# Kernel tuning notes

Hardware: AMD Instinct MI355X
Metric: run time of the kernel (lower is better)

The kernel has to match this reference:

```python
import jax, jax.numpy as jnp
import numpy as np

B, N, D, H = 4, 2048, 1024, 16
DK = D // H
LAMBDA = 0.5


def _linear_params(key, fan_in, fan_out):
    kw, kb = jax.random.split(key)
    bound = 1.0 / np.sqrt(fan_in)
    W = jax.random.uniform(kw, (fan_in, fan_out), jnp.float32, -bound, bound)
    b = jax.random.uniform(kb, (fan_out,), jnp.float32, -bound, bound)
    return W, b


def setup_inputs() -> dict:
    key = jax.random.key(0)
    ks = jax.random.split(key, 10)
    x = jax.random.normal(ks[0], (B, N, D), jnp.float32)
    # binary DAG-like adjacency (sparse-ish)
    causal_graph = jax.random.bernoulli(ks[1], 0.05, (N, N)).astype(jnp.float32)
    # differentiable backdoor mask: exp(-lambda*|Z|), 0 where no valid backdoor set
    Z = jax.random.randint(ks[2], (N, N), 0, 6).astype(jnp.float32)
    exists = jax.random.bernoulli(ks[3], 0.8, (N, N)).astype(jnp.float32)
    backdoor_mask = jnp.exp(-LAMBDA * Z) * exists
    Wq, bq = _linear_params(ks[4], D, D)
    Wk, bk = _linear_params(ks[5], D, D)
    Wc, bc = _linear_params(ks[6], N, D)  # W_cause: n_variables -> d_model
    We, be = _linear_params(ks[7], N, D)  # W_effect: n_variables -> d_model
    Wv, bv = _linear_params(ks[8], D, D)
    Wo, bo = _linear_params(ks[9], D, D)
    return dict(x=x, causal_graph=causal_graph, backdoor_mask=backdoor_mask,
                Wq=Wq, bq=bq, Wk=Wk, bk=bk, Wc=Wc, bc=bc, We=We, be=be,
                Wv=Wv, bv=bv, Wo=Wo, bo=bo)


def reference(x, causal_graph, backdoor_mask, Wq, bq, Wk, bk, Wc, bc, We, be, Wv, bv, Wo, bo):
    # Formula 5: asymmetric causal Q/K projections
    Q = x @ Wq + bq + (causal_graph @ Wc + bc)[None]        # [B,N,D]
    K = x @ Wk + bk + (causal_graph.T @ We + be)[None]      # [B,N,D]
    V = x @ Wv + bv                                          # [B,N,D]
    Qh = Q.reshape(B, N, H, DK)
    Kh = K.reshape(B, N, H, DK)
    Vh = V.reshape(B, N, H, DK)
    scores = jnp.einsum('bihd,bjhd->bhij', Qh, Kh) / np.sqrt(DK).astype(np.float32)
    # backdoor mask is MULTIPLICATIVE on raw scores (pre-softmax)
    scores = scores * backdoor_mask[None, None]
    attn = jax.nn.softmax(scores, axis=-1)                  # [B,H,N,N]
    out = jnp.einsum('bhij,bjhd->bihd', attn, Vh).reshape(B, N, D)
    return out @ Wo + bo
```

## Files before the change

kernel.cpp:

```cpp
#include <hip/hip_runtime.h>
#include <hip/hip_bf16.h>

#define BB 4
#define NN 2048
#define DD 1024
#define HH 16

using bf16 = __hip_bfloat16;
typedef __attribute__((ext_vector_type(8))) short bf16x8s;
typedef __attribute__((ext_vector_type(4))) float f32x4;

#define GLOAD_LDS16(gp, lp)                                                   \
  __builtin_amdgcn_global_load_lds(                                           \
      (const __attribute__((address_space(1))) void*)(gp),                    \
      (__attribute__((address_space(3))) void*)(lp), 16, 0, 0)

__global__ void cast_f32_bf16(const float* __restrict__ in, bf16* __restrict__ out, int n) {
  int i = (blockIdx.x * blockDim.x + threadIdx.x) * 4;
  if (i >= n) return;
  float4 v = *reinterpret_cast<const float4*>(in + i);
  ushort4 o;
  bf16 t0 = __float2bfloat16(v.x); o.x = *reinterpret_cast<unsigned short*>(&t0);
  bf16 t1 = __float2bfloat16(v.y); o.y = *reinterpret_cast<unsigned short*>(&t1);
  bf16 t2 = __float2bfloat16(v.z); o.z = *reinterpret_cast<unsigned short*>(&t2);
  bf16 t3 = __float2bfloat16(v.w); o.w = *reinterpret_cast<unsigned short*>(&t3);
  *reinterpret_cast<ushort4*>(out + i) = o;
}

__device__ __forceinline__ void transpose_tile(const float* __restrict__ in,
                                               bf16* __restrict__ out, int R, int C) {
  __shared__ float t[32][33];
  int c0 = blockIdx.x * 32, r0 = blockIdx.y * 32;
  int tx = threadIdx.x, ty = threadIdx.y;
#pragma unroll
  for (int i = 0; i < 4; i++)
    t[ty + i * 8][tx] = in[(size_t)(r0 + ty + i * 8) * C + c0 + tx];
  __syncthreads();
#pragma unroll
  for (int i = 0; i < 4; i++)
    out[(size_t)(c0 + ty + i * 8) * R + r0 + tx] = __float2bfloat16(t[tx][ty + i * 8]);
}

__global__ void transpose_cast4(const float* __restrict__ W0, const float* __restrict__ W1,
                                const float* __restrict__ W2, const float* __restrict__ W3,
                                bf16* __restrict__ O0, bf16* __restrict__ O1,
                                bf16* __restrict__ O2, bf16* __restrict__ O3) {
  const float* in; bf16* out;
  switch (blockIdx.z) {
    case 0: in = W0; out = O0; break;
    case 1: in = W1; out = O1; break;
    case 2: in = W2; out = O2; break;
    default: in = W3; out = O3; break;
  }
  transpose_tile(in, out, DD, DD);
}

__global__ void transpose_cast2(const float* __restrict__ W0, const float* __restrict__ W1,
                                bf16* __restrict__ O0, bf16* __restrict__ O1) {
  const float* in = blockIdx.z ? W1 : W0;
  bf16* out = blockIdx.z ? O1 : O0;
  transpose_tile(in, out, NN, DD);
}

__global__ void cg_prep(const float* __restrict__ in, bf16* __restrict__ outN,
                        bf16* __restrict__ outT) {
  __shared__ float t[32][33];
  int c0 = blockIdx.x * 32, r0 = blockIdx.y * 32;
  int tx = threadIdx.x, ty = threadIdx.y;
#pragma unroll
  for (int i = 0; i < 4; i++) {
    float v = in[(size_t)(r0 + ty + i * 8) * NN + c0 + tx];
    t[ty + i * 8][tx] = v;
    outN[(size_t)(r0 + ty + i * 8) * NN + c0 + tx] = __float2bfloat16(v);
  }
  __syncthreads();
#pragma unroll
  for (int i = 0; i < 4; i++)
    outT[(size_t)(c0 + ty + i * 8) * NN + r0 + tx] = __float2bfloat16(t[tx][ty + i * 8]);
}

__global__ void transpose_v(const bf16* __restrict__ Vb, bf16* __restrict__ Vt) {
  __shared__ short t[32][33];
  int bh = blockIdx.z; int b = bh >> 4, h = bh & 15;
  int n0 = blockIdx.x * 32, d0 = blockIdx.y * 32;
  int tx = threadIdx.x, ty = threadIdx.y;
#pragma unroll
  for (int i = 0; i < 4; i++)
    t[ty + i * 8][tx] = reinterpret_cast<const short*>(Vb)[
        (size_t)(b * NN + n0 + ty + i * 8) * DD + h * 64 + d0 + tx];
  __syncthreads();
#pragma unroll
  for (int i = 0; i < 4; i++)
    reinterpret_cast<short*>(Vt)[(size_t)(bh * 64 + d0 + ty + i * 8) * NN + n0 + tx] =
        t[tx][ty + i * 8];
}

template <int OUT_BF16, int HAS_ROWADD>
__device__ __forceinline__ void gemm_tile(
    const bf16* __restrict__ A, const bf16* __restrict__ BT, void* __restrict__ Cout,
    const float* __restrict__ bias, const float* __restrict__ rowadd,
    int Nc, int K, float scale, int brow, int bcol, short* As, short* Bs) {
  const int tid = threadIdx.x;
  const int l = tid & 63, w = tid >> 6;
  const int wr = (w >> 1) * 64, wc = (w & 1) * 64;
  const int lr = l & 15, lg = l >> 4;
  const int swz = lr & 7;
  f32x4 acc[4][4] = {};
  for (int k0 = 0; k0 < K; k0 += 64) {
#pragma unroll
    for (int i = 0; i < 4; i++) {
      int c = i * 256 + tid;
      int row = c >> 3, gch = (c & 7) ^ (row & 7);
      short* lA = As + (size_t)(i * 256 + w * 64) * 8;
      GLOAD_LDS16(A + (size_t)(brow + row) * K + k0 + gch * 8, lA);
      short* lB = Bs + (size_t)(i * 256 + w * 64) * 8;
      GLOAD_LDS16(BT + (size_t)(bcol + row) * K + k0 + gch * 8, lB);
    }
    __syncthreads();
#pragma unroll
    for (int t = 0; t < 2; t++) {
      bf16x8s a[4], bfr[4];
#pragma unroll
      for (int m = 0; m < 4; m++)
        a[m] = *reinterpret_cast<const bf16x8s*>(
            &As[(wr + m * 16 + lr) * 64 + ((t * 4 + lg) ^ swz) * 8]);
#pragma unroll
      for (int n = 0; n < 4; n++)
        bfr[n] = *reinterpret_cast<const bf16x8s*>(
            &Bs[(wc + n * 16 + lr) * 64 + ((t * 4 + lg) ^ swz) * 8]);
#pragma unroll
      for (int m = 0; m < 4; m++)
#pragma unroll
        for (int n = 0; n < 4; n++)
          acc[m][n] = __builtin_amdgcn_mfma_f32_16x16x32_bf16(a[m], bfr[n], acc[m][n], 0, 0, 0);
    }
    __syncthreads();
  }
#pragma unroll
  for (int m = 0; m < 4; m++) {
#pragma unroll
    for (int n = 0; n < 4; n++) {
      int col = bcol + wc + n * 16 + lr;
      float bv = bias[col];
#pragma unroll
      for (int r = 0; r < 4; r++) {
        int row = brow + wr + m * 16 + lg * 4 + r;
        float v = acc[m][n][r] + bv;
        if (HAS_ROWADD) v += rowadd[(size_t)(row & (NN - 1)) * Nc + col];
        v *= scale;
        if (OUT_BF16)
          reinterpret_cast<bf16*>(Cout)[(size_t)row * Nc + col] = __float2bfloat16(v);
        else
          reinterpret_cast<float*>(Cout)[(size_t)row * Nc + col] = v;
      }
    }
  }
}

template <int OUT_BF16, int HAS_ROWADD>
__global__ __launch_bounds__(256) void gemm_bt(
    const bf16* __restrict__ A, const bf16* __restrict__ BT, void* __restrict__ Cout,
    const float* __restrict__ bias, const float* __restrict__ rowadd,
    int M, int Nc, int K, float scale) {
  __shared__ short As[128 * 64];
  __shared__ short Bs[128 * 64];
  const int nbx = gridDim.x;
  const int nwg = nbx * gridDim.y;
  const int wg = blockIdx.y * nbx + blockIdx.x;
  const int swg = (wg & 7) * (nwg >> 3) + (wg >> 3);
  const int bxi = swg % nbx, byi = swg / nbx;
  gemm_tile<OUT_BF16, HAS_ROWADD>(A, BT, Cout, bias, rowadd, Nc, K, scale,
                                  byi * 128, bxi * 128, As, Bs);
}

__global__ __launch_bounds__(256) void gemm_dual(
    const bf16* __restrict__ A0, const bf16* __restrict__ B0, float* __restrict__ C0,
    const float* __restrict__ bias0,
    const bf16* __restrict__ A1, const bf16* __restrict__ B1, float* __restrict__ C1,
    const float* __restrict__ bias1, int Nc, int K) {
  __shared__ short As[128 * 64];
  __shared__ short Bs[128 * 64];
  const int nbx = gridDim.x;
  const int nwg = nbx * gridDim.y;
  const int wg = blockIdx.y * nbx + blockIdx.x;
  const int swg = (wg & 7) * (nwg >> 3) + (wg >> 3);
  const int bxi = swg % nbx, byi = swg / nbx;
  if (blockIdx.z == 0)
    gemm_tile<0, 0>(A0, B0, C0, bias0, nullptr, Nc, K, 1.0f, byi * 128, bxi * 128, As, Bs);
  else
    gemm_tile<0, 0>(A1, B1, C1, bias1, nullptr, Nc, K, 1.0f, byi * 128, bxi * 128, As, Bs);
}

__global__ __launch_bounds__(512, 4) void attn_k(
    const bf16* __restrict__ Qb, const bf16* __restrict__ Kb, const bf16* __restrict__ Vt,
    const float* __restrict__ mask, bf16* __restrict__ Ob) {
  constexpr int PPAD = 72;
  __shared__ short Ks[64 * 64];
  __shared__ short Vts[64 * 64];
  __shared__ short Ps[8][16 * PPAD];
  const int tid = threadIdx.x;
  const int wg = blockIdx.x;
  const int x = wg & 7, i = wg >> 3;
  const int b = x >> 1;
  const int h = ((x & 1) << 3) | (i & 7);
  const int q0 = ((i >> 3) & 15) * 128;
  const int l = tid & 63, w = tid >> 6;
  const int lr = l & 15, lg = l >> 4, lk = lg * 8;
  const int swz = lr & 7;

  const size_t qoff = (size_t)(b * NN + q0 + w * 16 + lr) * DD + h * 64;
  bf16x8s qf0 = *reinterpret_cast<const bf16x8s*>(Qb + qoff + lk);
  bf16x8s qf1 = *reinterpret_cast<const bf16x8s*>(Qb + qoff + 32 + lk);

  f32x4 acc[4] = {};
  float mrun = -1e30f, lrun = 0.f;

  const size_t kbase = (size_t)b * NN * DD + h * 64;
  const size_t vbase = (size_t)(b * HH + h) * 64 * NN;
  const float* mptr = mask + (size_t)(q0 + w * 16 + lr) * NN + lg * 4;

  const int r0 = tid >> 3, ch0 = tid & 7;
  const bf16* kg0 = Kb + kbase + (size_t)r0 * DD + ch0 * 8;
  const bf16* vg0 = Vt + vbase + (size_t)r0 * NN + ch0 * 8;
  short* kw0 = &Ks[r0 * 64 + (ch0 ^ (r0 & 7)) * 8];
  short* vw0 = &Vts[r0 * 64 + (ch0 ^ (r0 & 7)) * 8];

  uint4 kr0, vr0;
  kr0 = *reinterpret_cast<const uint4*>(kg0);
  vr0 = *reinterpret_cast<const uint4*>(vg0);

  for (int jt = 0; jt < NN; jt += 64) {
    __syncthreads();
    *reinterpret_cast<uint4*>(kw0) = kr0;
    *reinterpret_cast<uint4*>(vw0) = vr0;
    float4 m0 = *reinterpret_cast<const float4*>(mptr + jt + 0);
    float4 m1 = *reinterpret_cast<const float4*>(mptr + jt + 16);
    float4 m2 = *reinterpret_cast<const float4*>(mptr + jt + 32);
    float4 m3 = *reinterpret_cast<const float4*>(mptr + jt + 48);
    if (jt + 64 < NN) {
      kr0 = *reinterpret_cast<const uint4*>(kg0 + (size_t)(jt + 64) * DD);
      vr0 = *reinterpret_cast<const uint4*>(vg0 + jt + 64);
    }
    __syncthreads();

    f32x4 s[4];
#pragma unroll
    for (int jj = 0; jj < 4; jj++) {
      bf16x8s k0 = *reinterpret_cast<const bf16x8s*>(
          &Ks[(jj * 16 + lr) * 64 + ((0 + lg) ^ swz) * 8]);
      bf16x8s k1 = *reinterpret_cast<const bf16x8s*>(
          &Ks[(jj * 16 + lr) * 64 + ((4 + lg) ^ swz) * 8]);
      f32x4 z = {0.f, 0.f, 0.f, 0.f};
      z = __builtin_amdgcn_mfma_f32_16x16x32_bf16(k0, qf0, z, 0, 0, 0);
      s[jj] = __builtin_amdgcn_mfma_f32_16x16x32_bf16(k1, qf1, z, 0, 0, 0);
    }

    float lv[4][4];
    lv[0][0] = s[0][0] * m0.x; lv[0][1] = s[0][1] * m0.y;
    lv[0][2] = s[0][2] * m0.z; lv[0][3] = s[0][3] * m0.w;
    lv[1][0] = s[1][0] * m1.x; lv[1][1] = s[1][1] * m1.y;
    lv[1][2] = s[1][2] * m1.z; lv[1][3] = s[1][3] * m1.w;
    lv[2][0] = s[2][0] * m2.x; lv[2][1] = s[2][1] * m2.y;
    lv[2][2] = s[2][2] * m2.z; lv[2][3] = s[2][3] * m2.w;
    lv[3][0] = s[3][0] * m3.x; lv[3][1] = s[3][1] * m3.y;
    lv[3][2] = s[3][2] * m3.z; lv[3][3] = s[3][3] * m3.w;

    float mx0 = fmaxf(fmaxf(lv[0][0], lv[0][1]), fmaxf(lv[0][2], lv[0][3]));
    float mx1 = fmaxf(fmaxf(lv[1][0], lv[1][1]), fmaxf(lv[1][2], lv[1][3]));
    float mx2 = fmaxf(fmaxf(lv[2][0], lv[2][1]), fmaxf(lv[2][2], lv[2][3]));
    float mx3 = fmaxf(fmaxf(lv[3][0], lv[3][1]), fmaxf(lv[3][2], lv[3][3]));
    float mx = fmaxf(fmaxf(mx0, mx1), fmaxf(mx2, mx3));
    mx = fmaxf(mx, __shfl_xor(mx, 16, 64));
    mx = fmaxf(mx, __shfl_xor(mx, 32, 64));

    if (__any(mx > mrun + 11.0f)) {
      float mnew = fmaxf(mrun, mx);
      float sc = __builtin_amdgcn_exp2f(mrun - mnew);
      mrun = mnew;
      lrun *= sc;
#pragma unroll
      for (int s4 = 0; s4 < 4; s4++)
#pragma unroll
        for (int r = 0; r < 4; r++) acc[s4][r] *= sc;
    }

    short* Pw = &Ps[w][0];
    float rs = 0.f;
#pragma unroll
    for (int jj = 0; jj < 4; jj++) {
      float p0 = __builtin_amdgcn_exp2f(lv[jj][0] - mrun);
      float p1 = __builtin_amdgcn_exp2f(lv[jj][1] - mrun);
      float p2 = __builtin_amdgcn_exp2f(lv[jj][2] - mrun);
      float p3 = __builtin_amdgcn_exp2f(lv[jj][3] - mrun);
      rs += (p0 + p1) + (p2 + p3);
      ushort4 pk;
      bf16 b0 = __float2bfloat16(p0); pk.x = *reinterpret_cast<unsigned short*>(&b0);
      bf16 b1 = __float2bfloat16(p1); pk.y = *reinterpret_cast<unsigned short*>(&b1);
      bf16 b2 = __float2bfloat16(p2); pk.z = *reinterpret_cast<unsigned short*>(&b2);
      bf16 b3 = __float2bfloat16(p3); pk.w = *reinterpret_cast<unsigned short*>(&b3);
      *reinterpret_cast<ushort4*>(&Pw[lr * PPAD + jj * 16 + lg * 4]) = pk;
    }
    rs += __shfl_xor(rs, 16, 64);
    rs += __shfl_xor(rs, 32, 64);
    lrun += rs;

    asm volatile("s_waitcnt lgkmcnt(0)" ::: "memory");
    __builtin_amdgcn_sched_barrier(0);

    bf16x8s pb0 = *reinterpret_cast<const bf16x8s*>(&Pw[lr * PPAD + lk]);
    bf16x8s pb1 = *reinterpret_cast<const bf16x8s*>(&Pw[lr * PPAD + 32 + lk]);
#pragma unroll
    for (int s4 = 0; s4 < 4; s4++) {
      bf16x8s v0 = *reinterpret_cast<const bf16x8s*>(
          &Vts[(s4 * 16 + lr) * 64 + ((0 + lg) ^ swz) * 8]);
      bf16x8s v1 = *reinterpret_cast<const bf16x8s*>(
          &Vts[(s4 * 16 + lr) * 64 + ((4 + lg) ^ swz) * 8]);
      acc[s4] = __builtin_amdgcn_mfma_f32_16x16x32_bf16(v0, pb0, acc[s4], 0, 0, 0);
      acc[s4] = __builtin_amdgcn_mfma_f32_16x16x32_bf16(v1, pb1, acc[s4], 0, 0, 0);
    }
  }

  float rl = __builtin_amdgcn_rcpf(lrun);
  const size_t orow = (size_t)(b * NN + q0 + w * 16 + lr) * DD + h * 64;
#pragma unroll
  for (int s4 = 0; s4 < 4; s4++) {
    ushort4 o;
    bf16 b0 = __float2bfloat16(acc[s4][0] * rl); o.x = *reinterpret_cast<unsigned short*>(&b0);
    bf16 b1 = __float2bfloat16(acc[s4][1] * rl); o.y = *reinterpret_cast<unsigned short*>(&b1);
    bf16 b2 = __float2bfloat16(acc[s4][2] * rl); o.z = *reinterpret_cast<unsigned short*>(&b2);
    bf16 b3 = __float2bfloat16(acc[s4][3] * rl); o.w = *reinterpret_cast<unsigned short*>(&b3);
    *reinterpret_cast<ushort4*>(reinterpret_cast<unsigned short*>(Ob) + orow + s4 * 16 + lg * 4) = o;
  }
}

extern "C" void kernel_launch(void* const* d_in, const int* in_sizes, int n_in,
                              void* d_out, int out_size, void* d_ws, size_t ws_size,
                              hipStream_t stream) {
  (void)in_sizes; (void)n_in; (void)out_size; (void)ws_size;
  const float* x    = (const float*)d_in[0];
  const float* cg   = (const float*)d_in[1];
  const float* mask = (const float*)d_in[2];
  const float* Wq   = (const float*)d_in[3];
  const float* bq   = (const float*)d_in[4];
  const float* Wk   = (const float*)d_in[5];
  const float* bk   = (const float*)d_in[6];
  const float* Wc   = (const float*)d_in[7];
  const float* bc   = (const float*)d_in[8];
  const float* We   = (const float*)d_in[9];
  const float* be   = (const float*)d_in[10];
  const float* Wv   = (const float*)d_in[11];
  const float* bv   = (const float*)d_in[12];
  const float* Wo   = (const float*)d_in[13];
  const float* bo   = (const float*)d_in[14];

  auto MB = [](size_t m) { return m << 20; };
  char* ws = (char*)d_ws;
  bf16* xb   = (bf16*)(ws + MB(0));
  bf16* WqT  = (bf16*)(ws + MB(16));
  bf16* WkT  = (bf16*)(ws + MB(18));
  bf16* WvT  = (bf16*)(ws + MB(20));
  bf16* WoT  = (bf16*)(ws + MB(22));
  float* cq  = (float*)(ws + MB(24));
  float* ck  = (float*)(ws + MB(32));
  bf16* Qb   = (bf16*)(ws + MB(40));
  bf16* Kb   = (bf16*)(ws + MB(56));
  bf16* Vb   = (bf16*)(ws + MB(72));
  bf16* Vt   = (bf16*)(ws + MB(88));
  bf16* Ob   = (bf16*)(ws + MB(72));
  bf16* WcT  = (bf16*)(ws + MB(40));
  bf16* WeT  = (bf16*)(ws + MB(44));
  bf16* cgb  = (bf16*)(ws + MB(48));
  bf16* cgT  = (bf16*)(ws + MB(56));

  cast_f32_bf16<<<dim3(BB * NN * DD / 4 / 256), 256, 0, stream>>>(x, xb, BB * NN * DD);
  dim3 tb(32, 8);
  cg_prep<<<dim3(NN / 32, NN / 32), tb, 0, stream>>>(cg, cgb, cgT);
  transpose_cast4<<<dim3(DD / 32, DD / 32, 4), tb, 0, stream>>>(
      Wq, Wk, Wv, Wo, WqT, WkT, WvT, WoT);
  transpose_cast2<<<dim3(DD / 32, NN / 32, 2), tb, 0, stream>>>(Wc, We, WcT, WeT);

  gemm_dual<<<dim3(DD / 128, NN / 128, 2), 256, 0, stream>>>(
      cgb, WcT, cq, bc, cgT, WeT, ck, be, DD, NN);
  gemm_bt<1, 1><<<dim3(DD / 128, BB * NN / 128), 256, 0, stream>>>(
      xb, WqT, Qb, bq, cq, BB * NN, DD, DD, 0.125f * 1.4426950408889634f);
  gemm_bt<1, 1><<<dim3(DD / 128, BB * NN / 128), 256, 0, stream>>>(
      xb, WkT, Kb, bk, ck, BB * NN, DD, DD, 1.0f);
  gemm_bt<1, 0><<<dim3(DD / 128, BB * NN / 128), 256, 0, stream>>>(
      xb, WvT, Vb, bv, nullptr, BB * NN, DD, DD, 1.0f);

  transpose_v<<<dim3(NN / 32, 2, BB * HH), tb, 0, stream>>>(Vb, Vt);

  attn_k<<<dim3(NN / 128 * HH * BB), 512, 0, stream>>>(Qb, Kb, Vt, mask, Ob);

  gemm_bt<0, 0><<<dim3(DD / 128, BB * NN / 128), 256, 0, stream>>>(
      Ob, WoT, (float*)d_out, bo, nullptr, BB * NN, DD, DD, 1.0f);
}
```

Baseline: 310.8 us.

## Process two 16-row query tiles per wave in attention kernel

Each wave in the attention kernel now handles 32 query rows as two independent 16-row online-softmax streams, so each workgroup covers 256 queries and the grid is halved. Every K/V tile staged in shared memory is reused across twice as many queries, which cuts K/V global traffic and sync overhead per query. In exchange, register use roughly doubles (launch bounds drop from 4 to 2 waves-per-EU hint), occupancy falls, and there are only 512 workgroups.

Result: slower. 356.2 us (+14.6%).

```diff
diff --git a/kernel.cpp b/kernel.cpp
--- a/kernel.cpp
+++ b/kernel.cpp
@@ -191,33 +191,38 @@
     gemm_tile<0, 0>(A1, B1, C1, bias1, nullptr, Nc, K, 1.0f, byi * 128, bxi * 128, As, Bs);
 }
 
-__global__ __launch_bounds__(512, 4) void attn_k(
+__global__ __launch_bounds__(512, 2) void attn_k(
     const bf16* __restrict__ Qb, const bf16* __restrict__ Kb, const bf16* __restrict__ Vt,
     const float* __restrict__ mask, bf16* __restrict__ Ob) {
   constexpr int PPAD = 72;
   __shared__ short Ks[64 * 64];
   __shared__ short Vts[64 * 64];
-  __shared__ short Ps[8][16 * PPAD];
+  __shared__ short Ps[8][32 * PPAD];
   const int tid = threadIdx.x;
   const int wg = blockIdx.x;
   const int x = wg & 7, i = wg >> 3;
   const int b = x >> 1;
   const int h = ((x & 1) << 3) | (i & 7);
-  const int q0 = ((i >> 3) & 15) * 128;
+  const int q0 = ((i >> 3) & 7) * 256;
   const int l = tid & 63, w = tid >> 6;
   const int lr = l & 15, lg = l >> 4, lk = lg * 8;
   const int swz = lr & 7;
 
-  const size_t qoff = (size_t)(b * NN + q0 + w * 16 + lr) * DD + h * 64;
-  bf16x8s qf0 = *reinterpret_cast<const bf16x8s*>(Qb + qoff + lk);
-  bf16x8s qf1 = *reinterpret_cast<const bf16x8s*>(Qb + qoff + 32 + lk);
-
-  f32x4 acc[4] = {};
-  float mrun = -1e30f, lrun = 0.f;
+  const size_t qoffA = (size_t)(b * NN + q0 + w * 32 + lr) * DD + h * 64;
+  const size_t qoffB = qoffA + (size_t)16 * DD;
+  bf16x8s qf0a = *reinterpret_cast<const bf16x8s*>(Qb + qoffA + lk);
+  bf16x8s qf1a = *reinterpret_cast<const bf16x8s*>(Qb + qoffA + 32 + lk);
+  bf16x8s qf0b = *reinterpret_cast<const bf16x8s*>(Qb + qoffB + lk);
+  bf16x8s qf1b = *reinterpret_cast<const bf16x8s*>(Qb + qoffB + 32 + lk);
+
+  f32x4 accA[4] = {}, accB[4] = {};
+  float mrunA = -1e30f, lrunA = 0.f;
+  float mrunB = -1e30f, lrunB = 0.f;
 
   const size_t kbase = (size_t)b * NN * DD + h * 64;
   const size_t vbase = (size_t)(b * HH + h) * 64 * NN;
-  const float* mptr = mask + (size_t)(q0 + w * 16 + lr) * NN + lg * 4;
+  const float* mptrA = mask + (size_t)(q0 + w * 32 + lr) * NN + lg * 4;
+  const float* mptrB = mptrA + (size_t)16 * NN;
 
   const int r0 = tid >> 3, ch0 = tid & 7;
   const bf16* kg0 = Kb + kbase + (size_t)r0 * DD + ch0 * 8;
@@ -229,14 +234,16 @@
   kr0 = *reinterpret_cast<const uint4*>(kg0);
   vr0 = *reinterpret_cast<const uint4*>(vg0);
 
+  short* Pw = &Ps[w][0];
+
   for (int jt = 0; jt < NN; jt += 64) {
     __syncthreads();
     *reinterpret_cast<uint4*>(kw0) = kr0;
     *reinterpret_cast<uint4*>(vw0) = vr0;
-    float4 m0 = *reinterpret_cast<const float4*>(mptr + jt + 0);
-    float4 m1 = *reinterpret_cast<const float4*>(mptr + jt + 16);
-    float4 m2 = *reinterpret_cast<const float4*>(mptr + jt + 32);
-    float4 m3 = *reinterpret_cast<const float4*>(mptr + jt + 48);
+    float4 ma0 = *reinterpret_cast<const float4*>(mptrA + jt + 0);
+    float4 ma1 = *reinterpret_cast<const float4*>(mptrA + jt + 16);
+    float4 ma2 = *reinterpret_cast<const float4*>(mptrA + jt + 32);
+    float4 ma3 = *reinterpret_cast<const float4*>(mptrA + jt + 48);
     if (jt + 64 < NN) {
       kr0 = *reinterpret_cast<const uint4*>(kg0 + (size_t)(jt + 64) * DD);
       vr0 = *reinterpret_cast<const uint4*>(vg0 + jt + 64);
@@ -251,85 +258,154 @@
       bf16x8s k1 = *reinterpret_cast<const bf16x8s*>(
           &Ks[(jj * 16 + lr) * 64 + ((4 + lg) ^ swz) * 8]);
       f32x4 z = {0.f, 0.f, 0.f, 0.f};
-      z = __builtin_amdgcn_mfma_f32_16x16x32_bf16(k0, qf0, z, 0, 0, 0);
-      s[jj] = __builtin_amdgcn_mfma_f32_16x16x32_bf16(k1, qf1, z, 0, 0, 0);
-    }
+      z = __builtin_amdgcn_mfma_f32_16x16x32_bf16(k0, qf0a, z, 0, 0, 0);
+      s[jj] = __builtin_amdgcn_mfma_f32_16x16x32_bf16(k1, qf1a, z, 0, 0, 0);
+    }
+    float4 mb0 = *reinterpret_cast<const float4*>(mptrB + jt + 0);
+    float4 mb1 = *reinterpret_cast<const float4*>(mptrB + jt + 16);
+    float4 mb2 = *reinterpret_cast<const float4*>(mptrB + jt + 32);
+    float4 mb3 = *reinterpret_cast<const float4*>(mptrB + jt + 48);
 
     float lv[4][4];
-    lv[0][0] = s[0][0] * m0.x; lv[0][1] = s[0][1] * m0.y;
-    lv[0][2] = s[0][2] * m0.z; lv[0][3] = s[0][3] * m0.w;
-    lv[1][0] = s[1][0] * m1.x; lv[1][1] = s[1][1] * m1.y;
-    lv[1][2] = s[1][2] * m1.z; lv[1][3] = s[1][3] * m1.w;
-    lv[2][0] = s[2][0] * m2.x; lv[2][1] = s[2][1] * m2.y;
-    lv[2][2] = s[2][2] * m2.z; lv[2][3] = s[2][3] * m2.w;
-    lv[3][0] = s[3][0] * m3.x; lv[3][1] = s[3][1] * m3.y;
-    lv[3][2] = s[3][2] * m3.z; lv[3][3] = s[3][3] * m3.w;
-
-    float mx0 = fmaxf(fmaxf(lv[0][0], lv[0][1]), fmaxf(lv[0][2], lv[0][3]));
-    float mx1 = fmaxf(fmaxf(lv[1][0], lv[1][1]), fmaxf(lv[1][2], lv[1][3]));
-    float mx2 = fmaxf(fmaxf(lv[2][0], lv[2][1]), fmaxf(lv[2][2], lv[2][3]));
-    float mx3 = fmaxf(fmaxf(lv[3][0], lv[3][1]), fmaxf(lv[3][2], lv[3][3]));
-    float mx = fmaxf(fmaxf(mx0, mx1), fmaxf(mx2, mx3));
-    mx = fmaxf(mx, __shfl_xor(mx, 16, 64));
-    mx = fmaxf(mx, __shfl_xor(mx, 32, 64));
-
-    if (__any(mx > mrun + 11.0f)) {
-      float mnew = fmaxf(mrun, mx);
-      float sc = __builtin_amdgcn_exp2f(mrun - mnew);
-      mrun = mnew;
-      lrun *= sc;
-#pragma unroll
-      for (int s4 = 0; s4 < 4; s4++)
-#pragma unroll
-        for (int r = 0; r < 4; r++) acc[s4][r] *= sc;
-    }
-
-    short* Pw = &Ps[w][0];
-    float rs = 0.f;
+    lv[0][0] = s[0][0] * ma0.x; lv[0][1] = s[0][1] * ma0.y;
+    lv[0][2] = s[0][2] * ma0.z; lv[0][3] = s[0][3] * ma0.w;
+    lv[1][0] = s[1][0] * ma1.x; lv[1][1] = s[1][1] * ma1.y;
+    lv[1][2] = s[1][2] * ma1.z; lv[1][3] = s[1][3] * ma1.w;
+    lv[2][0] = s[2][0] * ma2.x; lv[2][1] = s[2][1] * ma2.y;
+    lv[2][2] = s[2][2] * ma2.z; lv[2][3] = s[2][3] * ma2.w;
+    lv[3][0] = s[3][0] * ma3.x; lv[3][1] = s[3][1] * ma3.y;
+    lv[3][2] = s[3][2] * ma3.z; lv[3][3] = s[3][3] * ma3.w;
+    {
+      float mx0 = fmaxf(fmaxf(lv[0][0], lv[0][1]), fmaxf(lv[0][2], lv[0][3]));
+      float mx1 = fmaxf(fmaxf(lv[1][0], lv[1][1]), fmaxf(lv[1][2], lv[1][3]));
+      float mx2 = fmaxf(fmaxf(lv[2][0], lv[2][1]), fmaxf(lv[2][2], lv[2][3]));
+      float mx3 = fmaxf(fmaxf(lv[3][0], lv[3][1]), fmaxf(lv[3][2], lv[3][3]));
+      float mx = fmaxf(fmaxf(mx0, mx1), fmaxf(mx2, mx3));
+      mx = fmaxf(mx, __shfl_xor(mx, 16, 64));
+      mx = fmaxf(mx, __shfl_xor(mx, 32, 64));
+      if (__any(mx > mrunA + 11.0f)) {
+        float mnew = fmaxf(mrunA, mx);
+        float sc = __builtin_amdgcn_exp2f(mrunA - mnew);
+        mrunA = mnew;
+        lrunA *= sc;
+#pragma unroll
+        for (int s4 = 0; s4 < 4; s4++)
+#pragma unroll
+          for (int r = 0; r < 4; r++) accA[s4][r] *= sc;
+      }
+      float rs = 0.f;
+#pragma unroll
+      for (int jj = 0; jj < 4; jj++) {
+        float p0 = __builtin_amdgcn_exp2f(lv[jj][0] - mrunA);
+        float p1 = __builtin_amdgcn_exp2f(lv[jj][1] - mrunA);
+        float p2 = __builtin_amdgcn_exp2f(lv[jj][2] - mrunA);
+        float p3 = __builtin_amdgcn_exp2f(lv[jj][3] - mrunA);
+        rs += (p0 + p1) + (p2 + p3);
+        ushort4 pk;
+        bf16 c0 = __float2bfloat16(p0); pk.x = *reinterpret_cast<unsigned short*>(&c0);
+        bf16 c1 = __float2bfloat16(p1); pk.y = *reinterpret_cast<unsigned short*>(&c1);
+        bf16 c2 = __float2bfloat16(p2); pk.z = *reinterpret_cast<unsigned short*>(&c2);
+        bf16 c3 = __float2bfloat16(p3); pk.w = *reinterpret_cast<unsigned short*>(&c3);
+        *reinterpret_cast<ushort4*>(&Pw[lr * PPAD + jj * 16 + lg * 4]) = pk;
+      }
+      rs += __shfl_xor(rs, 16, 64);
+      rs += __shfl_xor(rs, 32, 64);
+      lrunA += rs;
+    }
+
 #pragma unroll
     for (int jj = 0; jj < 4; jj++) {
-      float p0 = __builtin_amdgcn_exp2f(lv[jj][0] - mrun);
-      float p1 = __builtin_amdgcn_exp2f(lv[jj][1] - mrun);
-      float p2 = __builtin_amdgcn_exp2f(lv[jj][2] - mrun);
-      float p3 = __builtin_amdgcn_exp2f(lv[jj][3] - mrun);
-      rs += (p0 + p1) + (p2 + p3);
-      ushort4 pk;
-      bf16 b0 = __float2bfloat16(p0); pk.x = *reinterpret_cast<unsigned short*>(&b0);
-      bf16 b1 = __float2bfloat16(p1); pk.y = *reinterpret_cast<unsigned short*>(&b1);
-      bf16 b2 = __float2bfloat16(p2); pk.z = *reinterpret_cast<unsigned short*>(&b2);
-      bf16 b3 = __float2bfloat16(p3); pk.w = *reinterpret_cast<unsigned short*>(&b3);
-      *reinterpret_cast<ushort4*>(&Pw[lr * PPAD + jj * 16 + lg * 4]) = pk;
-    }
-    rs += __shfl_xor(rs, 16, 64);
-    rs += __shfl_xor(rs, 32, 64);
-    lrun += rs;
+      bf16x8s k0 = *reinterpret_cast<const bf16x8s*>(
+          &Ks[(jj * 16 + lr) * 64 + ((0 + lg) ^ swz) * 8]);
+      bf16x8s k1 = *reinterpret_cast<const bf16x8s*>(
+          &Ks[(jj * 16 + lr) * 64 + ((4 + lg) ^ swz) * 8]);
+      f32x4 z = {0.f, 0.f, 0.f, 0.f};
+      z = __builtin_amdgcn_mfma_f32_16x16x32_bf16(k0, qf0b, z, 0, 0, 0);
+      s[jj] = __builtin_amdgcn_mfma_f32_16x16x32_bf16(k1, qf1b, z, 0, 0, 0);
+    }
+    lv[0][0] = s[0][0] * mb0.x; lv[0][1] = s[0][1] * mb0.y;
+    lv[0][2] = s[0][2] * mb0.z; lv[0][3] = s[0][3] * mb0.w;
+    lv[1][0] = s[1][0] * mb1.x; lv[1][1] = s[1][1] * mb1.y;
+    lv[1][2] = s[1][2] * mb1.z; lv[1][3] = s[1][3] * mb1.w;
+    lv[2][0] = s[2][0] * mb2.x; lv[2][1] = s[2][1] * mb2.y;
+    lv[2][2] = s[2][2] * mb2.z; lv[2][3] = s[2][3] * mb2.w;
+    lv[3][0] = s[3][0] * mb3.x; lv[3][1] = s[3][1] * mb3.y;
+    lv[3][2] = s[3][2] * mb3.z; lv[3][3] = s[3][3] * mb3.w;
+    {
+      float mx0 = fmaxf(fmaxf(lv[0][0], lv[0][1]), fmaxf(lv[0][2], lv[0][3]));
+      float mx1 = fmaxf(fmaxf(lv[1][0], lv[1][1]), fmaxf(lv[1][2], lv[1][3]));
+      float mx2 = fmaxf(fmaxf(lv[2][0], lv[2][1]), fmaxf(lv[2][2], lv[2][3]));
+      float mx3 = fmaxf(fmaxf(lv[3][0], lv[3][1]), fmaxf(lv[3][2], lv[3][3]));
+      float mx = fmaxf(fmaxf(mx0, mx1), fmaxf(mx2, mx3));
+      mx = fmaxf(mx, __shfl_xor(mx, 16, 64));
+      mx = fmaxf(mx, __shfl_xor(mx, 32, 64));
+      if (__any(mx > mrunB + 11.0f)) {
+        float mnew = fmaxf(mrunB, mx);
+        float sc = __builtin_amdgcn_exp2f(mrunB - mnew);
+        mrunB = mnew;
+        lrunB *= sc;
+#pragma unroll
+        for (int s4 = 0; s4 < 4; s4++)
+#pragma unroll
+          for (int r = 0; r < 4; r++) accB[s4][r] *= sc;
+      }
+      float rs = 0.f;
+#pragma unroll
+      for (int jj = 0; jj < 4; jj++) {
+        float p0 = __builtin_amdgcn_exp2f(lv[jj][0] - mrunB);
+        float p1 = __builtin_amdgcn_exp2f(lv[jj][1] - mrunB);
+        float p2 = __builtin_amdgcn_exp2f(lv[jj][2] - mrunB);
+        float p3 = __builtin_amdgcn_exp2f(lv[jj][3] - mrunB);
+        rs += (p0 + p1) + (p2 + p3);
+        ushort4 pk;
+        bf16 c0 = __float2bfloat16(p0); pk.x = *reinterpret_cast<unsigned short*>(&c0);
+        bf16 c1 = __float2bfloat16(p1); pk.y = *reinterpret_cast<unsigned short*>(&c1);
+        bf16 c2 = __float2bfloat16(p2); pk.z = *reinterpret_cast<unsigned short*>(&c2);
+        bf16 c3 = __float2bfloat16(p3); pk.w = *reinterpret_cast<unsigned short*>(&c3);
+        *reinterpret_cast<ushort4*>(&Pw[(16 + lr) * PPAD + jj * 16 + lg * 4]) = pk;
+      }
+      rs += __shfl_xor(rs, 16, 64);
+      rs += __shfl_xor(rs, 32, 64);
+      lrunB += rs;
+    }
 
     asm volatile("s_waitcnt lgkmcnt(0)" ::: "memory");
     __builtin_amdgcn_sched_barrier(0);
 
-    bf16x8s pb0 = *reinterpret_cast<const bf16x8s*>(&Pw[lr * PPAD + lk]);
-    bf16x8s pb1 = *reinterpret_cast<const bf16x8s*>(&Pw[lr * PPAD + 32 + lk]);
+    bf16x8s pb0a = *reinterpret_cast<const bf16x8s*>(&Pw[lr * PPAD + lk]);
+    bf16x8s pb1a = *reinterpret_cast<const bf16x8s*>(&Pw[lr * PPAD + 32 + lk]);
+    bf16x8s pb0b = *reinterpret_cast<const bf16x8s*>(&Pw[(16 + lr) * PPAD + lk]);
+    bf16x8s pb1b = *reinterpret_cast<const bf16x8s*>(&Pw[(16 + lr) * PPAD + 32 + lk]);
 #pragma unroll
     for (int s4 = 0; s4 < 4; s4++) {
       bf16x8s v0 = *reinterpret_cast<const bf16x8s*>(
           &Vts[(s4 * 16 + lr) * 64 + ((0 + lg) ^ swz) * 8]);
       bf16x8s v1 = *reinterpret_cast<const bf16x8s*>(
           &Vts[(s4 * 16 + lr) * 64 + ((4 + lg) ^ swz) * 8]);
-      acc[s4] = __builtin_amdgcn_mfma_f32_16x16x32_bf16(v0, pb0, acc[s4], 0, 0, 0);
-      acc[s4] = __builtin_amdgcn_mfma_f32_16x16x32_bf16(v1, pb1, acc[s4], 0, 0, 0);
-    }
-  }
-
-  float rl = __builtin_amdgcn_rcpf(lrun);
-  const size_t orow = (size_t)(b * NN + q0 + w * 16 + lr) * DD + h * 64;
+      accA[s4] = __builtin_amdgcn_mfma_f32_16x16x32_bf16(v0, pb0a, accA[s4], 0, 0, 0);
+      accA[s4] = __builtin_amdgcn_mfma_f32_16x16x32_bf16(v1, pb1a, accA[s4], 0, 0, 0);
+      accB[s4] = __builtin_amdgcn_mfma_f32_16x16x32_bf16(v0, pb0b, accB[s4], 0, 0, 0);
+      accB[s4] = __builtin_amdgcn_mfma_f32_16x16x32_bf16(v1, pb1b, accB[s4], 0, 0, 0);
+    }
+  }
+
+  float rlA = __builtin_amdgcn_rcpf(lrunA);
+  float rlB = __builtin_amdgcn_rcpf(lrunB);
+  const size_t orowA = (size_t)(b * NN + q0 + w * 32 + lr) * DD + h * 64;
+  const size_t orowB = orowA + (size_t)16 * DD;
 #pragma unroll
   for (int s4 = 0; s4 < 4; s4++) {
     ushort4 o;
-    bf16 b0 = __float2bfloat16(acc[s4][0] * rl); o.x = *reinterpret_cast<unsigned short*>(&b0);
-    bf16 b1 = __float2bfloat16(acc[s4][1] * rl); o.y = *reinterpret_cast<unsigned short*>(&b1);
-    bf16 b2 = __float2bfloat16(acc[s4][2] * rl); o.z = *reinterpret_cast<unsigned short*>(&b2);
-    bf16 b3 = __float2bfloat16(acc[s4][3] * rl); o.w = *reinterpret_cast<unsigned short*>(&b3);
-    *reinterpret_cast<ushort4*>(reinterpret_cast<unsigned short*>(Ob) + orow + s4 * 16 + lg * 4) = o;
+    bf16 c0 = __float2bfloat16(accA[s4][0] * rlA); o.x = *reinterpret_cast<unsigned short*>(&c0);
+    bf16 c1 = __float2bfloat16(accA[s4][1] * rlA); o.y = *reinterpret_cast<unsigned short*>(&c1);
+    bf16 c2 = __float2bfloat16(accA[s4][2] * rlA); o.z = *reinterpret_cast<unsigned short*>(&c2);
+    bf16 c3 = __float2bfloat16(accA[s4][3] * rlA); o.w = *reinterpret_cast<unsigned short*>(&c3);
+    *reinterpret_cast<ushort4*>(reinterpret_cast<unsigned short*>(Ob) + orowA + s4 * 16 + lg * 4) = o;
+    bf16 d0 = __float2bfloat16(accB[s4][0] * rlB); o.x = *reinterpret_cast<unsigned short*>(&d0);
+    bf16 d1 = __float2bfloat16(accB[s4][1] * rlB); o.y = *reinterpret_cast<unsigned short*>(&d1);
+    bf16 d2 = __float2bfloat16(accB[s4][2] * rlB); o.z = *reinterpret_cast<unsigned short*>(&d2);
+    bf16 d3 = __float2bfloat16(accB[s4][3] * rlB); o.w = *reinterpret_cast<unsigned short*>(&d3);
+    *reinterpret_cast<ushort4*>(reinterpret_cast<unsigned short*>(Ob) + orowB + s4 * 16 + lg * 4) = o;
   }
 }
 
@@ -390,7 +466,7 @@
 
   transpose_v<<<dim3(NN / 32, 2, BB * HH), tb, 0, stream>>>(Vb, Vt);
 
-  attn_k<<<dim3(NN / 128 * HH * BB), 512, 0, stream>>>(Qb, Kb, Vt, mask, Ob);
+  attn_k<<<dim3(NN / 256 * HH * BB), 512, 0, stream>>>(Qb, Kb, Vt, mask, Ob);
 
   gemm_bt<0, 0><<<dim3(DD / 128, BB * NN / 128), 256, 0, stream>>>(
       Ob, WoT, (float*)d_out, bo, nullptr, BB * NN, DD, DD, 1.0f);
```
